# Optimization experiments

Measured on AMD Instinct MI355X. Metric: run time of the kernel, lower is better.

The kernel has to match this reference:

```python
import jax, jax.numpy as jnp
import numpy as np

E, D, H, T = 8, 2048, 5632, 32768  # experts, dim, hidden_dim, total routed tokens


def setup_inputs() -> dict:
    key = jax.random.key(0)
    k_x, k1, k2, k3 = jax.random.split(key, 4)
    x = jax.random.normal(k_x, (T, D), dtype=jnp.float32)
    # trunc_normal init stds per init_weights (approx: plain normal, same scale)
    std = (2.0 / (D * 24)) ** 0.5
    w1 = jax.random.normal(k1, (E, H, D), dtype=jnp.float32) * std
    w2 = jax.random.normal(k2, (E, D, H), dtype=jnp.float32) * std
    w3 = jax.random.normal(k3, (E, H, D), dtype=jnp.float32) * std
    # tokens are pre-sorted by expert; even split 4096 tokens/expert (sums to T)
    num_tokens_per_expert = jnp.full((E,), T // E, dtype=jnp.int32)
    return {"x": x, "w1": w1, "w2": w2, "w3": w3,
            "num_tokens_per_expert": num_tokens_per_expert}


def _grouped_experts(x, w1, w2, w3, counts):
    # Faithful to _run_experts_grouped_mm: grouped GEMMs computed in bf16,
    # SwiGLU activation, cast back to x dtype.
    xb = x.astype(jnp.bfloat16)
    w1b = jnp.transpose(w1.astype(jnp.bfloat16), (0, 2, 1))  # [E, D, H]
    w3b = jnp.transpose(w3.astype(jnp.bfloat16), (0, 2, 1))  # [E, D, H]
    w2b = jnp.transpose(w2.astype(jnp.bfloat16), (0, 2, 1))  # [E, H, D]
    h1 = jax.lax.ragged_dot(xb, w1b, counts)   # [T, H]
    h3 = jax.lax.ragged_dot(xb, w3b, counts)   # [T, H]
    h = jax.nn.silu(h1) * h3                   # fused SwiGLU gate
    out = jax.lax.ragged_dot(h, w2b, counts)   # [T, D]
    return out.astype(x.dtype)


def reference(x, w1, w2, w3, num_tokens_per_expert):
    return _grouped_experts(x, w1, w2, w3, num_tokens_per_expert)
```

## Files before the change

### kernel.cpp

```cpp
#include <hip/hip_runtime.h>
#include <hip/hip_bf16.h>
#include <stdint.h>

#define TT 32768
#define DD 2048
#define HH 5632
#define NE 8

typedef __bf16 bf16;
typedef __bf16 bf16x8 __attribute__((ext_vector_type(8)));
typedef float  f32x4  __attribute__((ext_vector_type(4)));

__device__ __forceinline__ void gl16(const void* g, void* l) {
    __builtin_amdgcn_global_load_lds(
        (const __attribute__((address_space(1))) void*)g,
        (__attribute__((address_space(3))) void*)l, 16, 0, 0);
}
#define VMW(n) asm volatile("s_waitcnt vmcnt(" #n ")" ::: "memory")
#define LGKM0() do { asm volatile("s_waitcnt lgkmcnt(0)" ::: "memory"); \
                     __builtin_amdgcn_sched_barrier(0); } while (0)
#define BARRIER() __builtin_amdgcn_s_barrier()

__device__ __forceinline__ int swz(int off) { return off ^ (((off >> 7) & 3) << 4); }

__device__ __forceinline__ int expert_of(const int* counts, int row0) {
    int base = 0;
    for (int i = 0; i < NE; ++i) { int c = counts[i]; if (row0 < base + c) return i; base += c; }
    return NE - 1;
}

__global__ __launch_bounds__(256)
void k_cvt(const float* __restrict__ in, bf16* __restrict__ out, long n) {
    long i = ((long)blockIdx.x * 256 + threadIdx.x) * 8;
    const long stride = (long)gridDim.x * 256 * 8;
    for (; i < n; i += stride) {
        const float4* p = (const float4*)(in + i);
        float4 a = p[0], b = p[1];
        union { bf16 v[8]; uint4 u; } r;
        r.v[0] = (bf16)a.x; r.v[1] = (bf16)a.y; r.v[2] = (bf16)a.z; r.v[3] = (bf16)a.w;
        r.v[4] = (bf16)b.x; r.v[5] = (bf16)b.y; r.v[6] = (bf16)b.z; r.v[7] = (bf16)b.w;
        *(uint4*)(out + i) = r.u;
    }
}

#define M1_LOAD(t1, NA, NB1, NB3) do {                                        \
    const char* nb_ = sm + (size_t)((t1) % 5) * 32768;                        \
    _Pragma("unroll")                                                         \
    for (int mi = 0; mi < 8; ++mi)                                            \
        NA[mi] = *(const bf16x8*)(nb_ + aoff0 + mi * 1024);                   \
    _Pragma("unroll")                                                         \
    for (int ni = 0; ni < 2; ++ni) {                                          \
        NB1[ni] = *(const bf16x8*)(nb_ + 16384 + boff0 + ni * 1024);          \
        NB3[ni] = *(const bf16x8*)(nb_ + 24576 + boff0 + ni * 1024);          \
    }                                                                         \
    __builtin_amdgcn_sched_barrier(0);                                        \
} while (0)

#define M1_ITER(t, CA, CB1, CB3, NA, NB1, NB3) do {                           \
    if ((t) + 4 < NT) { stage((t) + 4); VMW(8); }                             \
    else if ((t) == NT - 4) { VMW(4); }                                       \
    else if ((t) == NT - 3) { VMW(0); }                                       \
    LGKM0();                                                                  \
    if ((t) + 1 < NT) M1_LOAD((t) + 1, NA, NB1, NB3);                         \
    __builtin_amdgcn_s_setprio(1);                                            \
    _Pragma("unroll")                                                         \
    for (int mi = 0; mi < 8; ++mi)                                            \
    _Pragma("unroll")                                                         \
    for (int ni = 0; ni < 2; ++ni) {                                          \
        acc1[mi][ni] = __builtin_amdgcn_mfma_f32_16x16x32_bf16(CA[mi], CB1[ni], acc1[mi][ni], 0, 0, 0); \
        acc3[mi][ni] = __builtin_amdgcn_mfma_f32_16x16x32_bf16(CA[mi], CB3[ni], acc3[mi][ni], 0, 0, 0); \
    }                                                                         \
    __builtin_amdgcn_s_setprio(0);                                            \
    BARRIER();                                                                \
} while (0)

__global__ __launch_bounds__(512, 2)
void k_moe1(const bf16* __restrict__ xb, const bf16* __restrict__ w1b,
            const bf16* __restrict__ w3b, const int* __restrict__ counts,
            bf16* __restrict__ h) {
    extern __shared__ __align__(16) char sm[];
    const int tid = threadIdx.x;
    const int nwg = gridDim.x;
    const int cpx = nwg >> 3;
    const int c   = blockIdx.x & 7;
    const int local = blockIdx.x >> 3;
    const int nt = local >> 4;
    const int mt = (c << 4) + (local & 15);
    const int row0 = mt * 256, col0 = nt * 128;
    const int e = expert_of(counts, row0);
    (void)cpx;

    const char *sa0, *sa1, *sa2, *sa3;
    {
        int off0 = tid * 16, off1 = 8192 + tid * 16;
        int s0 = swz(off0), s1 = swz(off1);
        sa0 = (const char*)xb + (((size_t)(row0 + (s0 >> 6)) * DD) << 1) + (s0 & 63);
        sa1 = (const char*)xb + (((size_t)(row0 + (s1 >> 6)) * DD) << 1) + (s1 & 63);
        const char* w1p = (const char*)(w1b + (size_t)e * HH * DD);
        const char* w3p = (const char*)(w3b + (size_t)e * HH * DD);
        sa2 = w1p + (((size_t)(col0 + (s0 >> 6)) * DD) << 1) + (s0 & 63);
        sa3 = w3p + (((size_t)(col0 + (s0 >> 6)) * DD) << 1) + (s0 & 63);
    }
    const int dst0 = tid * 16;

    auto stage = [&](int kt) {
        char* db = sm + (size_t)(kt % 5) * 32768;
        const size_t ko = (size_t)kt << 6;
        gl16(sa0 + ko, db + dst0);
        gl16(sa1 + ko, db + 8192 + dst0);
        gl16(sa2 + ko, db + 16384 + dst0);
        gl16(sa3 + ko, db + 24576 + dst0);
    };

    const int lane = tid & 63, wv = tid >> 6;
    const int wrow = wv >> 2, wcol = wv & 3;
    const int lrow = lane & 15, kb = (lane >> 4) << 4;

    const int aoff0 = swz((wrow * 128 + lrow) * 64 + kb);
    const int boff0 = swz((wcol * 32 + lrow) * 64 + kb);

    f32x4 acc1[8][2] = {};
    f32x4 acc3[8][2] = {};
    bf16x8 Xa[8], Xb1[2], Xb3[2], Ya[8], Yb1[2], Yb3[2];

    const int NT = DD / 32;
    stage(0); stage(1); stage(2); stage(3);
    VMW(8);
    BARRIER();
    M1_LOAD(0, Xa, Xb1, Xb3);
    for (int t = 0; t < NT; t += 2) {
        M1_ITER(t,     Xa, Xb1, Xb3, Ya, Yb1, Yb3);
        M1_ITER(t + 1, Ya, Yb1, Yb3, Xa, Xb1, Xb3);
    }

#pragma unroll
    for (int mi = 0; mi < 8; ++mi)
#pragma unroll
        for (int ni = 0; ni < 2; ++ni)
#pragma unroll
            for (int j = 0; j < 4; ++j) {
                int row = row0 + wrow * 128 + mi * 16 + ((lane >> 4) << 2) + j;
                int col = col0 + wcol * 32 + ni * 16 + lrow;
                float f1 = (float)(bf16)acc1[mi][ni][j];
                float f3 = (float)(bf16)acc3[mi][ni][j];
                float s = f1 / (1.0f + __expf(-f1));
                h[(size_t)row * HH + col] = (bf16)(s * f3);
            }
}

#define G2_LOAD(t1, NA, NB) do {                                              \
    const char* nb_ = sm + (size_t)((t1) % 5) * 32768;                        \
    _Pragma("unroll")                                                         \
    for (int mi = 0; mi < 8; ++mi)                                            \
        NA[mi] = *(const bf16x8*)(nb_ + aoff0 + mi * 1024);                   \
    _Pragma("unroll")                                                         \
    for (int ni = 0; ni < 4; ++ni)                                            \
        NB[ni] = *(const bf16x8*)(nb_ + 16384 + boff0 + ni * 1024);           \
    __builtin_amdgcn_sched_barrier(0);                                        \
} while (0)

#define G2_ITER(t, CA, CB, NA, NB) do {                                       \
    if ((t) + 4 < NT) { stage((t) + 4); VMW(8); }                             \
    else if ((t) == NT - 4) { VMW(4); }                                       \
    else if ((t) == NT - 3) { VMW(0); }                                       \
    LGKM0();                                                                  \
    if ((t) + 1 < NT) G2_LOAD((t) + 1, NA, NB);                               \
    __builtin_amdgcn_s_setprio(1);                                            \
    _Pragma("unroll")                                                         \
    for (int mi = 0; mi < 8; ++mi)                                            \
    _Pragma("unroll")                                                         \
    for (int ni = 0; ni < 4; ++ni)                                            \
        acc[mi][ni] = __builtin_amdgcn_mfma_f32_16x16x32_bf16(CA[mi], CB[ni], acc[mi][ni], 0, 0, 0); \
    __builtin_amdgcn_s_setprio(0);                                            \
    BARRIER();                                                                \
} while (0)

__global__ __launch_bounds__(512, 2)
void k_g2(const bf16* __restrict__ hb, const bf16* __restrict__ w2b,
          const int* __restrict__ counts, float* __restrict__ out) {
    extern __shared__ __align__(16) char sm[];
    const int tid = threadIdx.x;
    const int nwg = gridDim.x;
    int wg = blockIdx.x;
    wg = (wg & 7) * (nwg >> 3) + (wg >> 3);
    const int NTN = DD / 256;
    const int mt = wg / NTN, nt = wg - mt * NTN;
    const int row0 = mt * 256, col0 = nt * 256;
    const int e = expert_of(counts, row0);

    const char *sa0, *sa1, *sa2, *sa3;
    {
        int off0 = tid * 16, off1 = 8192 + tid * 16;
        int s0 = swz(off0), s1 = swz(off1);
        sa0 = (const char*)hb + (((size_t)(row0 + (s0 >> 6)) * HH) << 1) + (s0 & 63);
        sa1 = (const char*)hb + (((size_t)(row0 + (s1 >> 6)) * HH) << 1) + (s1 & 63);
        const char* wp = (const char*)(w2b + (size_t)e * DD * HH);
        sa2 = wp + (((size_t)(col0 + (s0 >> 6)) * HH) << 1) + (s0 & 63);
        sa3 = wp + (((size_t)(col0 + (s1 >> 6)) * HH) << 1) + (s1 & 63);
    }
    const int dst0 = tid * 16;
    auto stage = [&](int kt) {
        char* db = sm + (size_t)(kt % 5) * 32768;
        const size_t ko = (size_t)kt << 6;
        gl16(sa0 + ko, db + dst0);
        gl16(sa1 + ko, db + 8192 + dst0);
        gl16(sa2 + ko, db + 16384 + dst0);
        gl16(sa3 + ko, db + 24576 + dst0);
    };

    const int lane = tid & 63, wv = tid >> 6;
    const int wrow = wv >> 2, wcol = wv & 3;
    const int lrow = lane & 15, kb = (lane >> 4) << 4;

    const int aoff0 = swz((wrow * 128 + lrow) * 64 + kb);
    const int boff0 = swz((wcol * 64 + lrow) * 64 + kb);

    f32x4 acc[8][4] = {};
    bf16x8 Xa[8], Xb[4], Ya[8], Yb[4];

    const int NT = HH / 32;
    stage(0); stage(1); stage(2); stage(3);
    VMW(8);
    BARRIER();
    G2_LOAD(0, Xa, Xb);
    for (int t = 0; t < NT; t += 2) {
        G2_ITER(t,     Xa, Xb, Ya, Yb);
        G2_ITER(t + 1, Ya, Yb, Xa, Xb);
    }

#pragma unroll
    for (int mi = 0; mi < 8; ++mi)
#pragma unroll
        for (int ni = 0; ni < 4; ++ni)
#pragma unroll
            for (int j = 0; j < 4; ++j) {
                int row = row0 + wrow * 128 + mi * 16 + ((lane >> 4) << 2) + j;
                int col = col0 + wcol * 64 + ni * 16 + lrow;
                out[(size_t)row * DD + col] = (float)(bf16)acc[mi][ni][j];
            }
}

extern "C" void kernel_launch(void* const* d_in, const int* in_sizes, int n_in,
                              void* d_out, int out_size, void* d_ws, size_t ws_size,
                              hipStream_t stream) {
    const float* x      = (const float*)d_in[0];
    const float* w1     = (const float*)d_in[1];
    const float* w2     = (const float*)d_in[2];
    const float* w3     = (const float*)d_in[3];
    const int*   counts = (const int*)d_in[4];
    float* out = (float*)d_out;

    const size_t xb_b = (size_t)TT * DD * 2;
    const size_t h_b  = (size_t)TT * HH * 2;
    const size_t w_b  = (size_t)NE * HH * DD * 2;
    const size_t need_full = xb_b + h_b + 2 * w_b;
    if (ws_size < need_full) return;

    bf16* xb  = (bf16*)d_ws;
    bf16* h   = (bf16*)((char*)d_ws + xb_b);
    bf16* wsA = (bf16*)((char*)d_ws + xb_b + h_b);
    bf16* wsB = (bf16*)((char*)d_ws + xb_b + h_b + w_b);

    hipFuncSetAttribute((const void*)k_moe1, hipFuncAttributeMaxDynamicSharedMemorySize, 163840);
    hipFuncSetAttribute((const void*)k_g2,   hipFuncAttributeMaxDynamicSharedMemorySize, 163840);

    k_cvt<<<2048, 256, 0, stream>>>(x,  xb,  (long)TT * DD);
    k_cvt<<<2048, 256, 0, stream>>>(w1, wsA, (long)NE * HH * DD);
    k_cvt<<<2048, 256, 0, stream>>>(w3, wsB, (long)NE * HH * DD);
    k_moe1<<<(HH / 128) * (TT / 256), 512, 163840, stream>>>(xb, wsA, wsB, counts, h);
    k_cvt<<<2048, 256, 0, stream>>>(w2, wsA, (long)NE * DD * HH);
    k_g2<<<(DD / 256) * (TT / 256), 512, 163840, stream>>>(h, wsA, counts, out);
}
```

Before: 2.659 ms.

## Make GEMM kernels persistent with cross-tile continuous load pipeline

```diff
diff --git a/kernel.cpp b/kernel.cpp
--- a/kernel.cpp
+++ b/kernel.cpp
@@ -43,8 +43,8 @@
     }
 }
 
-#define M1_LOAD(t1, NA, NB1, NB3) do {                                        \
-    const char* nb_ = sm + (size_t)((t1) % 5) * 32768;                        \
+#define M1_LOAD(bufb, NA, NB1, NB3) do {                                      \
+    const char* nb_ = sm + (bufb);                                            \
     _Pragma("unroll")                                                         \
     for (int mi = 0; mi < 8; ++mi)                                            \
         NA[mi] = *(const bf16x8*)(nb_ + aoff0 + mi * 1024);                   \
@@ -56,12 +56,12 @@
     __builtin_amdgcn_sched_barrier(0);                                        \
 } while (0)
 
-#define M1_ITER(t, CA, CB1, CB3, NA, NB1, NB3) do {                           \
-    if ((t) + 4 < NT) { stage((t) + 4); VMW(8); }                             \
-    else if ((t) == NT - 4) { VMW(4); }                                       \
-    else if ((t) == NT - 3) { VMW(0); }                                       \
+#define M1_ITER(g, bLb, bSb, ko, CA, CB1, CB3, NA, NB1, NB3) do {             \
+    if ((g) + 4 < GTOT) { stage((ko), (bSb)); VMW(8); }                       \
+    else if ((g) == GTOT - 4) { VMW(4); }                                     \
+    else if ((g) == GTOT - 3) { VMW(0); }                                     \
     LGKM0();                                                                  \
-    if ((t) + 1 < NT) M1_LOAD((t) + 1, NA, NB1, NB3);                         \
+    if ((g) + 1 < GTOT) M1_LOAD((bLb), NA, NB1, NB3);                         \
     __builtin_amdgcn_s_setprio(1);                                            \
     _Pragma("unroll")                                                         \
     for (int mi = 0; mi < 8; ++mi)                                            \
@@ -80,32 +80,34 @@
             bf16* __restrict__ h) {
     extern __shared__ __align__(16) char sm[];
     const int tid = threadIdx.x;
-    const int nwg = gridDim.x;
-    const int cpx = nwg >> 3;
-    const int c   = blockIdx.x & 7;
-    const int local = blockIdx.x >> 3;
-    const int nt = local >> 4;
-    const int mt = (c << 4) + (local & 15);
-    const int row0 = mt * 256, col0 = nt * 128;
-    const int e = expert_of(counts, row0);
-    (void)cpx;
+    const int c = blockIdx.x & 7;
+    const int j = blockIdx.x >> 3;
+    const int NSEG = 22;
+    const int NT = 64;
+    const int GTOT = NSEG * NT;
+
+    const int s0 = swz(tid * 16);
+    const int s1 = 8192 + s0;
+    const int dst0 = tid * 16;
 
     const char *sa0, *sa1, *sa2, *sa3;
-    {
-        int off0 = tid * 16, off1 = 8192 + tid * 16;
-        int s0 = swz(off0), s1 = swz(off1);
-        sa0 = (const char*)xb + (((size_t)(row0 + (s0 >> 6)) * DD) << 1) + (s0 & 63);
-        sa1 = (const char*)xb + (((size_t)(row0 + (s1 >> 6)) * DD) << 1) + (s1 & 63);
+    int sseg = 0;
+    auto set_bases = [&](int sg) {
+        int local = sg * 32 + j;
+        int r0 = ((c << 4) + (local & 15)) * 256;
+        int c0 = (local >> 4) * 128;
+        int e = expert_of(counts, r0);
+        sa0 = (const char*)xb + (((size_t)(r0 + (s0 >> 6)) * DD) << 1) + (s0 & 63);
+        sa1 = (const char*)xb + (((size_t)(r0 + (s1 >> 6)) * DD) << 1) + (s1 & 63);
         const char* w1p = (const char*)(w1b + (size_t)e * HH * DD);
         const char* w3p = (const char*)(w3b + (size_t)e * HH * DD);
-        sa2 = w1p + (((size_t)(col0 + (s0 >> 6)) * DD) << 1) + (s0 & 63);
-        sa3 = w3p + (((size_t)(col0 + (s0 >> 6)) * DD) << 1) + (s0 & 63);
-    }
-    const int dst0 = tid * 16;
-
-    auto stage = [&](int kt) {
-        char* db = sm + (size_t)(kt % 5) * 32768;
-        const size_t ko = (size_t)kt << 6;
+        sa2 = w1p + (((size_t)(c0 + (s0 >> 6)) * DD) << 1) + (s0 & 63);
+        sa3 = w3p + (((size_t)(c0 + (s0 >> 6)) * DD) << 1) + (s0 & 63);
+    };
+    set_bases(0);
+
+    auto stage = [&](int ko, int bufb) {
+        char* db = sm + bufb;
         gl16(sa0 + ko, db + dst0);
         gl16(sa1 + ko, db + 8192 + dst0);
         gl16(sa2 + ko, db + 16384 + dst0);
@@ -115,7 +117,6 @@
     const int lane = tid & 63, wv = tid >> 6;
     const int wrow = wv >> 2, wcol = wv & 3;
     const int lrow = lane & 15, kb = (lane >> 4) << 4;
-
     const int aoff0 = swz((wrow * 128 + lrow) * 64 + kb);
     const int boff0 = swz((wcol * 32 + lrow) * 64 + kb);
 
@@ -123,33 +124,60 @@
     f32x4 acc3[8][2] = {};
     bf16x8 Xa[8], Xb1[2], Xb3[2], Ya[8], Yb1[2], Yb3[2];
 
-    const int NT = DD / 32;
-    stage(0); stage(1); stage(2); stage(3);
+    stage(0, 0); stage(64, 32768); stage(128, 65536); stage(192, 98304);
     VMW(8);
     BARRIER();
     M1_LOAD(0, Xa, Xb1, Xb3);
-    for (int t = 0; t < NT; t += 2) {
-        M1_ITER(t,     Xa, Xb1, Xb3, Ya, Yb1, Yb3);
-        M1_ITER(t + 1, Ya, Yb1, Yb3, Xa, Xb1, Xb3);
+
+    int tc = 0;
+    int stk = 256;
+    int b0 = 0;
+    int cseg = 0;
+    int crow0 = ((c << 4) + (j & 15)) * 256;
+    int ccol0 = (j >> 4) * 128;
+
+    for (int gp = 0; gp < GTOT; gp += 2) {
+        int bL1 = b0 + 1; if (bL1 >= 5) bL1 -= 5;
+        int bL2 = b0 + 2; if (bL2 >= 5) bL2 -= 5;
+        int bS1 = b0 + 4; if (bS1 >= 5) bS1 -= 5;
+        const int bS2 = b0;
+        if (tc == 60 && sseg + 1 < NSEG) { ++sseg; set_bases(sseg); stk = 0; }
+
+        M1_ITER(gp,     bL1 << 15, bS1 << 15, stk,      Xa, Xb1, Xb3, Ya, Yb1, Yb3);
+        M1_ITER(gp + 1, bL2 << 15, bS2 << 15, stk + 64, Ya, Yb1, Yb3, Xa, Xb1, Xb3);
+        stk += 128;
+        b0 += 2; if (b0 >= 5) b0 -= 5;
+
+        if (tc == 62) {
+#pragma unroll
+            for (int mi = 0; mi < 8; ++mi)
+#pragma unroll
+                for (int ni = 0; ni < 2; ++ni) {
+#pragma unroll
+                    for (int jj = 0; jj < 4; ++jj) {
+                        int row = crow0 + wrow * 128 + mi * 16 + ((lane >> 4) << 2) + jj;
+                        int col = ccol0 + wcol * 32 + ni * 16 + lrow;
+                        float f1 = (float)(bf16)acc1[mi][ni][jj];
+                        float f3 = (float)(bf16)acc3[mi][ni][jj];
+                        float s = f1 / (1.0f + __expf(-f1));
+                        h[(size_t)row * HH + col] = (bf16)(s * f3);
+                    }
+                    acc1[mi][ni] = (f32x4){0.f, 0.f, 0.f, 0.f};
+                    acc3[mi][ni] = (f32x4){0.f, 0.f, 0.f, 0.f};
+                }
+            ++cseg;
+            int local = cseg * 32 + j;
+            crow0 = ((c << 4) + (local & 15)) * 256;
+            ccol0 = (local >> 4) * 128;
+            tc = 0;
+        } else {
+            tc += 2;
+        }
     }
-
-#pragma unroll
-    for (int mi = 0; mi < 8; ++mi)
-#pragma unroll
-        for (int ni = 0; ni < 2; ++ni)
-#pragma unroll
-            for (int j = 0; j < 4; ++j) {
-                int row = row0 + wrow * 128 + mi * 16 + ((lane >> 4) << 2) + j;
-                int col = col0 + wcol * 32 + ni * 16 + lrow;
-                float f1 = (float)(bf16)acc1[mi][ni][j];
-                float f3 = (float)(bf16)acc3[mi][ni][j];
-                float s = f1 / (1.0f + __expf(-f1));
-                h[(size_t)row * HH + col] = (bf16)(s * f3);
-            }
-}
-
-#define G2_LOAD(t1, NA, NB) do {                                              \
-    const char* nb_ = sm + (size_t)((t1) % 5) * 32768;                        \
+}
+
+#define G2_LOAD(bufb, NA, NB) do {                                            \
+    const char* nb_ = sm + (bufb);                                            \
     _Pragma("unroll")                                                         \
     for (int mi = 0; mi < 8; ++mi)                                            \
         NA[mi] = *(const bf16x8*)(nb_ + aoff0 + mi * 1024);                   \
@@ -159,12 +187,12 @@
     __builtin_amdgcn_sched_barrier(0);                                        \
 } while (0)
 
-#define G2_ITER(t, CA, CB, NA, NB) do {                                       \
-    if ((t) + 4 < NT) { stage((t) + 4); VMW(8); }                             \
-    else if ((t) == NT - 4) { VMW(4); }                                       \
-    else if ((t) == NT - 3) { VMW(0); }                                       \
+#define G2_ITER(g, bLb, bSb, ko, CA, CB, NA, NB) do {                         \
+    if ((g) + 4 < GTOT) { stage((ko), (bSb)); VMW(8); }                       \
+    else if ((g) == GTOT - 4) { VMW(4); }                                     \
+    else if ((g) == GTOT - 3) { VMW(0); }                                     \
     LGKM0();                                                                  \
-    if ((t) + 1 < NT) G2_LOAD((t) + 1, NA, NB);                               \
+    if ((g) + 1 < GTOT) G2_LOAD((bLb), NA, NB);                               \
     __builtin_amdgcn_s_setprio(1);                                            \
     _Pragma("unroll")                                                         \
     for (int mi = 0; mi < 8; ++mi)                                            \
@@ -180,28 +208,33 @@
           const int* __restrict__ counts, float* __restrict__ out) {
     extern __shared__ __align__(16) char sm[];
     const int tid = threadIdx.x;
-    const int nwg = gridDim.x;
-    int wg = blockIdx.x;
-    wg = (wg & 7) * (nwg >> 3) + (wg >> 3);
-    const int NTN = DD / 256;
-    const int mt = wg / NTN, nt = wg - mt * NTN;
-    const int row0 = mt * 256, col0 = nt * 256;
-    const int e = expert_of(counts, row0);
+    const int c = blockIdx.x & 7;
+    const int j = blockIdx.x >> 3;
+    const int NSEG = 4;
+    const int NT = 176;
+    const int GTOT = NSEG * NT;
+
+    const int s0 = swz(tid * 16);
+    const int s1 = 8192 + s0;
+    const int dst0 = tid * 16;
 
     const char *sa0, *sa1, *sa2, *sa3;
-    {
-        int off0 = tid * 16, off1 = 8192 + tid * 16;
-        int s0 = swz(off0), s1 = swz(off1);
-        sa0 = (const char*)hb + (((size_t)(row0 + (s0 >> 6)) * HH) << 1) + (s0 & 63);
-        sa1 = (const char*)hb + (((size_t)(row0 + (s1 >> 6)) * HH) << 1) + (s1 & 63);
+    int sseg = 0;
+    auto set_bases = [&](int sg) {
+        int local = sg * 32 + j;
+        int r0 = ((c << 4) + (local & 15)) * 256;
+        int c0 = (local >> 4) * 256;
+        int e = expert_of(counts, r0);
+        sa0 = (const char*)hb + (((size_t)(r0 + (s0 >> 6)) * HH) << 1) + (s0 & 63);
+        sa1 = (const char*)hb + (((size_t)(r0 + (s1 >> 6)) * HH) << 1) + (s1 & 63);
         const char* wp = (const char*)(w2b + (size_t)e * DD * HH);
-        sa2 = wp + (((size_t)(col0 + (s0 >> 6)) * HH) << 1) + (s0 & 63);
-        sa3 = wp + (((size_t)(col0 + (s1 >> 6)) * HH) << 1) + (s1 & 63);
-    }
-    const int dst0 = tid * 16;
-    auto stage = [&](int kt) {
-        char* db = sm + (size_t)(kt % 5) * 32768;
-        const size_t ko = (size_t)kt << 6;
+        sa2 = wp + (((size_t)(c0 + (s0 >> 6)) * HH) << 1) + (s0 & 63);
+        sa3 = wp + (((size_t)(c0 + (s1 >> 6)) * HH) << 1) + (s1 & 63);
+    };
+    set_bases(0);
+
+    auto stage = [&](int ko, int bufb) {
+        char* db = sm + bufb;
         gl16(sa0 + ko, db + dst0);
         gl16(sa1 + ko, db + 8192 + dst0);
         gl16(sa2 + ko, db + 16384 + dst0);
@@ -211,33 +244,56 @@
     const int lane = tid & 63, wv = tid >> 6;
     const int wrow = wv >> 2, wcol = wv & 3;
     const int lrow = lane & 15, kb = (lane >> 4) << 4;
-
     const int aoff0 = swz((wrow * 128 + lrow) * 64 + kb);
     const int boff0 = swz((wcol * 64 + lrow) * 64 + kb);
 
     f32x4 acc[8][4] = {};
     bf16x8 Xa[8], Xb[4], Ya[8], Yb[4];
 
-    const int NT = HH / 32;
-    stage(0); stage(1); stage(2); stage(3);
+    stage(0, 0); stage(64, 32768); stage(128, 65536); stage(192, 98304);
     VMW(8);
     BARRIER();
     G2_LOAD(0, Xa, Xb);
-    for (int t = 0; t < NT; t += 2) {
-        G2_ITER(t,     Xa, Xb, Ya, Yb);
-        G2_ITER(t + 1, Ya, Yb, Xa, Xb);
+
+    int tc = 0, stk = 256, b0 = 0;
+    int cseg = 0;
+    int crow0 = ((c << 4) + (j & 15)) * 256;
+    int ccol0 = (j >> 4) * 256;
+
+    for (int gp = 0; gp < GTOT; gp += 2) {
+        int bL1 = b0 + 1; if (bL1 >= 5) bL1 -= 5;
+        int bL2 = b0 + 2; if (bL2 >= 5) bL2 -= 5;
+        int bS1 = b0 + 4; if (bS1 >= 5) bS1 -= 5;
+        const int bS2 = b0;
+        if (tc == 172 && sseg + 1 < NSEG) { ++sseg; set_bases(sseg); stk = 0; }
+
+        G2_ITER(gp,     bL1 << 15, bS1 << 15, stk,      Xa, Xb, Ya, Yb);
+        G2_ITER(gp + 1, bL2 << 15, bS2 << 15, stk + 64, Ya, Yb, Xa, Xb);
+        stk += 128;
+        b0 += 2; if (b0 >= 5) b0 -= 5;
+
+        if (tc == 174) {
+#pragma unroll
+            for (int mi = 0; mi < 8; ++mi)
+#pragma unroll
+                for (int ni = 0; ni < 4; ++ni) {
+#pragma unroll
+                    for (int jj = 0; jj < 4; ++jj) {
+                        int row = crow0 + wrow * 128 + mi * 16 + ((lane >> 4) << 2) + jj;
+                        int col = ccol0 + wcol * 64 + ni * 16 + lrow;
+                        out[(size_t)row * DD + col] = (float)(bf16)acc[mi][ni][jj];
+                    }
+                    acc[mi][ni] = (f32x4){0.f, 0.f, 0.f, 0.f};
+                }
+            ++cseg;
+            int local = cseg * 32 + j;
+            crow0 = ((c << 4) + (local & 15)) * 256;
+            ccol0 = (local >> 4) * 256;
+            tc = 0;
+        } else {
+            tc += 2;
+        }
     }
-
-#pragma unroll
-    for (int mi = 0; mi < 8; ++mi)
-#pragma unroll
-        for (int ni = 0; ni < 4; ++ni)
-#pragma unroll
-            for (int j = 0; j < 4; ++j) {
-                int row = row0 + wrow * 128 + mi * 16 + ((lane >> 4) << 2) + j;
-                int col = col0 + wcol * 64 + ni * 16 + lrow;
-                out[(size_t)row * DD + col] = (float)(bf16)acc[mi][ni][j];
-            }
 }
 
 extern "C" void kernel_launch(void* const* d_in, const int* in_sizes, int n_in,
@@ -267,7 +323,7 @@
     k_cvt<<<2048, 256, 0, stream>>>(x,  xb,  (long)TT * DD);
     k_cvt<<<2048, 256, 0, stream>>>(w1, wsA, (long)NE * HH * DD);
     k_cvt<<<2048, 256, 0, stream>>>(w3, wsB, (long)NE * HH * DD);
-    k_moe1<<<(HH / 128) * (TT / 256), 512, 163840, stream>>>(xb, wsA, wsB, counts, h);
+    k_moe1<<<256, 512, 163840, stream>>>(xb, wsA, wsB, counts, h);
     k_cvt<<<2048, 256, 0, stream>>>(w2, wsA, (long)NE * DD * HH);
-    k_g2<<<(DD / 256) * (TT / 256), 512, 163840, stream>>>(h, wsA, counts, out);
-}
+    k_g2<<<256, 512, 163840, stream>>>(h, wsA, counts, out);
+}
```

Measured after the change: 3.174 ms. 19.4% more time.
